# Kernel tuning notes

Measured on AMD Instinct MI355X. Metric: run time of the kernel, lower is better.

## Reference

```python
import jax, jax.numpy as jnp
import numpy as np

B, S, IN_DIM = 8, 4096, 1024
H, D = 16, 64          # num_heads, head_dim (attention_dim = H*D = 1024)
OUT_DIM = 1024
EPS = 1e-6
HI = jax.lax.Precision.HIGHEST


def setup_inputs() -> dict:
    key = jax.random.key(0)
    ks = jax.random.split(key, 9)
    sx = 1.0 / np.sqrt(IN_DIM)
    so = 1.0 / np.sqrt(H * D)
    return {
        "x":  jax.random.normal(ks[0], (B, S, IN_DIM), jnp.float32),
        "wq": jax.random.normal(ks[1], (IN_DIM, H, D), jnp.float32) * sx,
        "bq": jnp.zeros((H, D), jnp.float32),
        "wk": jax.random.normal(ks[2], (IN_DIM, H, D), jnp.float32) * sx,
        "bk": jnp.zeros((H, D), jnp.float32),
        "wv": jax.random.normal(ks[3], (IN_DIM, H, D), jnp.float32) * sx,
        "bv": jnp.zeros((H, D), jnp.float32),
        "wo": jax.random.normal(ks[4], (H, D, OUT_DIM), jnp.float32) * so,
        "bo": jnp.zeros((OUT_DIM,), jnp.float32),
    }


def _feature_map(t):
    return jax.nn.elu(t) + 1.0


def reference(x, wq, bq, wk, bk, wv, bv, wo, bo):
    # QKV projections: [B,S,IN] x [IN,H,D] -> [B,S,H,D]
    q = jnp.einsum('bsi,ihd->bshd', x, wq) + bq
    k = jnp.einsum('bsi,ihd->bshd', x, wk) + bk
    v = jnp.einsum('bsi,ihd->bshd', x, wv) + bv

    Q = _feature_map(q)
    K = _feature_map(k)

    # Faithful to source: KV is an elementwise K*V reduced over seq -> [B,H,D]
    KV = jnp.einsum('bshd,bshd->bhd', K, v, precision=HI)
    Ksum = jnp.sum(K, axis=1)                      # [B,H,D]
    Z = 1.0 / (Q * Ksum[:, None, :, :] + EPS)      # [B,S,H,D]
    attn = Q * KV[:, None, :, :] * Z               # [B,S,H,D]

    # output projection contracts heads and head_dim
    out = jnp.einsum('bshd,hdo->bso', attn, wo) + bo
    return jax.nn.gelu(out)  # flax default gelu is approximate=True
```

## Files before the change

### kernel.cpp

```cpp
#include <hip/hip_runtime.h>


#define SEQ   4096
#define MROWS 32768
#define KDIM  1024
#define HD    1024
#define T32   32

typedef __bf16 bf16x8 __attribute__((ext_vector_type(8)));
typedef float floatx4 __attribute__((ext_vector_type(4)));

__device__ __forceinline__ unsigned short f2bf(float f) {
    unsigned int u = __float_as_uint(f);
    u += 0x7fffu + ((u >> 16) & 1u);
    return (unsigned short)(u >> 16);
}
__device__ __forceinline__ void cvt8(const float* __restrict__ p, unsigned short* d) {
    const float4 a = *(const float4*)p;
    const float4 b = *(const float4*)(p + 4);
    d[0] = f2bf(a.x); d[1] = f2bf(a.y); d[2] = f2bf(a.z); d[3] = f2bf(a.w);
    d[4] = f2bf(b.x); d[5] = f2bf(b.y); d[6] = f2bf(b.z); d[7] = f2bf(b.w);
}

typedef const __attribute__((address_space(1))) unsigned int* gas_t;
typedef __attribute__((address_space(3))) unsigned int* las_t;
__device__ __forceinline__ void async16(const void* g, void* l) {
    __builtin_amdgcn_global_load_lds((gas_t)g, (las_t)l, 16, 0, 0);
}

__global__ __launch_bounds__(256)
void cvt_x(const float* __restrict__ x, unsigned short* __restrict__ xb)
{
    const size_t p = ((size_t)blockIdx.x * 256 + threadIdx.x) * 8;
    union { uint4 u; unsigned short s[8]; } o;
    cvt8(x + p, o.s);
    *(uint4*)(xb + p) = o.u;
}

__global__ __launch_bounds__(256)
void transpose_w(const float* __restrict__ wk, const float* __restrict__ wv,
                 unsigned short* __restrict__ wkT, unsigned short* __restrict__ wvT)
{
    __shared__ alignas(16) unsigned short Ts[64][72];
    const float* W = blockIdx.z ? wv : wk;
    unsigned short* WT = blockIdx.z ? wvT : wkT;
    const int k0 = blockIdx.x * 64, n0 = blockIdx.y * 64;
    const int t = threadIdx.x;
    const int r4 = (t >> 4) * 4, c4 = (t & 15) * 4;
#pragma unroll
    for (int i = 0; i < 4; i++) {
        const float4 f = *(const float4*)(W + (size_t)(k0 + r4 + i) * HD + n0 + c4);
        Ts[c4 + 0][r4 + i] = f2bf(f.x);
        Ts[c4 + 1][r4 + i] = f2bf(f.y);
        Ts[c4 + 2][r4 + i] = f2bf(f.z);
        Ts[c4 + 3][r4 + i] = f2bf(f.w);
    }
    __syncthreads();
    const int rr = t >> 3, cc = (t & 7) * 8;
#pragma unroll
    for (int h = 0; h < 2; h++)
        *(uint4*)(WT + (size_t)(n0 + rr + h * 32) * KDIM + k0 + cc) =
            *(const uint4*)&Ts[rr + h * 32][cc];
}

__global__ __launch_bounds__(512, 1)
void kv_gemm_fast(const unsigned short* __restrict__ xb,
                  const unsigned short* __restrict__ wkT,
                  const unsigned short* __restrict__ wvT,
                  const float* __restrict__ bk, const float* __restrict__ bv,
                  float2* __restrict__ KVZ)
{
    __shared__ alignas(16) unsigned short As[4][256 * 32];
    __shared__ alignas(16) unsigned short Bs[4][256 * 32];

    const int t = threadIdx.x;

    const int id = blockIdx.x;
    const int xcd = id & 7, o = id >> 3;
    const int mtile = xcd * 16 + (o >> 3);
    const int ntile = o & 7;
    const int m0 = mtile * 256;
    const int n0 = ntile * 128;
    const int b  = m0 >> 12;

    const int w = t >> 6, lane = t & 63;
    const int wm = w >> 1, wn = w & 1;
    const int lrow = lane & 15, quad = lane >> 4;

    const int usw = quad ^ ((lrow >> 1) & 3);

    const int srow  = t >> 2;
    const int usrc  = (t & 3) ^ ((t >> 3) & 3);
    const unsigned short* gA0 = xb  + (size_t)(m0 + srow) * KDIM + usrc * 8;
    const unsigned short* gA1 = gA0 + (size_t)128 * KDIM;
    const unsigned short* gBk = wkT + (size_t)(n0 + srow) * KDIM + usrc * 8;
    const unsigned short* gBv = wvT + (size_t)(n0 + srow) * KDIM + usrc * 8;

#define STAGE(c, tk) do {                                                     \
        const int ko_ = (tk) * 32;                                            \
        async16(gA0 + ko_, &As[c][(0 * 512 + t) * 8]);                        \
        async16(gA1 + ko_, &As[c][(1 * 512 + t) * 8]);                        \
        async16(gBk + ko_, &Bs[c][(0 * 512 + t) * 8]);                        \
        async16(gBv + ko_, &Bs[c][(1 * 512 + t) * 8]);                        \
    } while (0)

    STAGE(0, 0);
    STAGE(1, 1);
    STAGE(2, 2);

    floatx4 accK[4][4], accV[4][4];
#pragma unroll
    for (int i = 0; i < 4; i++)
#pragma unroll
        for (int j = 0; j < 4; j++) {
            accK[i][j] = (floatx4){0.f, 0.f, 0.f, 0.f};
            accV[i][j] = (floatx4){0.f, 0.f, 0.f, 0.f};
        }

    asm volatile("s_waitcnt vmcnt(8)" ::: "memory");
    __builtin_amdgcn_s_barrier();

    for (int tk = 0; tk < T32; ++tk) {
        const unsigned short* A = As[tk & 3];
        const unsigned short* B = Bs[tk & 3];

        bf16x8 af[4], bK[4], bV[4];
#pragma unroll
        for (int mi = 0; mi < 4; ++mi)
            af[mi] = *(const bf16x8*)&A[(wm * 64 + mi * 16 + lrow) * 32 + usw * 8];
#pragma unroll
        for (int ni = 0; ni < 4; ++ni) {
            const int br = wn * 64 + ni * 16 + lrow;
            bK[ni] = *(const bf16x8*)&B[ br        * 32 + usw * 8];
            bV[ni] = *(const bf16x8*)&B[(br + 128) * 32 + usw * 8];
        }

        __builtin_amdgcn_s_setprio(1);
#pragma unroll
        for (int mi = 0; mi < 4; ++mi)
#pragma unroll
            for (int ni = 0; ni < 4; ++ni) {
                accK[mi][ni] = __builtin_amdgcn_mfma_f32_16x16x32_bf16(
                    af[mi], bK[ni], accK[mi][ni], 0, 0, 0);
                accV[mi][ni] = __builtin_amdgcn_mfma_f32_16x16x32_bf16(
                    af[mi], bV[ni], accV[mi][ni], 0, 0, 0);
            }
        __builtin_amdgcn_s_setprio(0);

        if (tk + 3 < T32) {
            STAGE((tk + 3) & 3, tk + 3);
            asm volatile("s_waitcnt vmcnt(8)" ::: "memory");
        } else if (tk == T32 - 3) {
            asm volatile("s_waitcnt vmcnt(4)" ::: "memory");
        } else if (tk == T32 - 2) {
            asm volatile("s_waitcnt vmcnt(0)" ::: "memory");
        }
        __builtin_amdgcn_s_barrier();
    }
#undef STAGE

#pragma unroll
    for (int ni = 0; ni < 4; ++ni) {
        const int colw = n0 + wn * 64 + ni * 16 + lrow;
        const float bkf = bk[colw];
        const float bvf = bv[colw];
        float pKV = 0.f, pK = 0.f;
#pragma unroll
        for (int mi = 0; mi < 4; ++mi) {
#pragma unroll
            for (int r = 0; r < 4; ++r) {
                const float kk = accK[mi][ni][r] + bkf;
                const float K  = (kk > 0.f) ? (kk + 1.f) : __expf(kk);
                const float vv = accV[mi][ni][r] + bvf;
                pKV += K * vv;
                pK  += K;
            }
        }
        pKV += __shfl_xor(pKV, 16, 64);
        pKV += __shfl_xor(pKV, 32, 64);
        pK  += __shfl_xor(pK, 16, 64);
        pK  += __shfl_xor(pK, 32, 64);
        if (quad == 0) {
            atomicAdd(&KVZ[b * HD + colw].x, pKV);
            atomicAdd(&KVZ[b * HD + colw].y, pK);
        }
    }
}

__global__ __launch_bounds__(256)
void kv_gemm(const float* __restrict__ x,
             const float* __restrict__ wk, const float* __restrict__ bk,
             const float* __restrict__ wv, const float* __restrict__ bv,
             float2* __restrict__ KVZ)
{
    __shared__ alignas(16) unsigned short As [128][40];
    __shared__ alignas(16) unsigned short BsK[128][40];
    __shared__ alignas(16) unsigned short BsV[128][40];

    const int t = threadIdx.x;
    const int n0 = blockIdx.x * 128;
    const int m0 = blockIdx.y * 128;
    const int b  = m0 >> 12;

    const int wave = t >> 6, lane = t & 63;
    const int wm = wave >> 1, wn = wave & 1;
    const int lrow = lane & 15, quad = lane >> 4;

    floatx4 accK[4][4], accV[4][4];
#pragma unroll
    for (int i = 0; i < 4; i++)
#pragma unroll
        for (int j = 0; j < 4; j++) {
            accK[i][j] = (floatx4){0.f, 0.f, 0.f, 0.f};
            accV[i][j] = (floatx4){0.f, 0.f, 0.f, 0.f};
        }

    const int arow0 = t >> 2, akc = (t & 3) * 8;
    const int bk0 = t >> 4, bnc = (t & 15) * 8;

    for (int k0 = 0; k0 < KDIM; k0 += 32) {
        __syncthreads();
        {
            union { uint4 u; unsigned short s[8]; } ua, ub;
            cvt8(x + (size_t)(m0 + arow0) * KDIM + k0 + akc, ua.s);
            cvt8(x + (size_t)(m0 + arow0 + 64) * KDIM + k0 + akc, ub.s);
            *(uint4*)&As[arow0][akc] = ua.u;
            *(uint4*)&As[arow0 + 64][akc] = ub.u;
        }
        {
            unsigned short k0s[8], k1s[8], v0s[8], v1s[8];
            cvt8(wk + (size_t)(k0 + bk0) * HD + n0 + bnc, k0s);
            cvt8(wk + (size_t)(k0 + bk0 + 16) * HD + n0 + bnc, k1s);
            cvt8(wv + (size_t)(k0 + bk0) * HD + n0 + bnc, v0s);
            cvt8(wv + (size_t)(k0 + bk0 + 16) * HD + n0 + bnc, v1s);
#pragma unroll
            for (int j = 0; j < 8; j++) {
                BsK[bnc + j][bk0]      = k0s[j];
                BsK[bnc + j][bk0 + 16] = k1s[j];
                BsV[bnc + j][bk0]      = v0s[j];
                BsV[bnc + j][bk0 + 16] = v1s[j];
            }
        }
        __syncthreads();

        bf16x8 af[4], bfK[4], bfV[4];
#pragma unroll
        for (int mi = 0; mi < 4; mi++)
            af[mi] = *(const bf16x8*)&As[wm * 64 + mi * 16 + lrow][quad * 8];
#pragma unroll
        for (int ni = 0; ni < 4; ni++) {
            bfK[ni] = *(const bf16x8*)&BsK[wn * 64 + ni * 16 + lrow][quad * 8];
            bfV[ni] = *(const bf16x8*)&BsV[wn * 64 + ni * 16 + lrow][quad * 8];
        }
#pragma unroll
        for (int mi = 0; mi < 4; mi++)
#pragma unroll
            for (int ni = 0; ni < 4; ni++) {
                accK[mi][ni] = __builtin_amdgcn_mfma_f32_16x16x32_bf16(
                    af[mi], bfK[ni], accK[mi][ni], 0, 0, 0);
                accV[mi][ni] = __builtin_amdgcn_mfma_f32_16x16x32_bf16(
                    af[mi], bfV[ni], accV[mi][ni], 0, 0, 0);
            }
    }

#pragma unroll
    for (int ni = 0; ni < 4; ni++) {
        const int colw = n0 + wn * 64 + ni * 16 + lrow;
        const float bkf = bk[colw];
        const float bvf = bv[colw];
        float pKV = 0.f, pK = 0.f;
#pragma unroll
        for (int mi = 0; mi < 4; mi++) {
#pragma unroll
            for (int r = 0; r < 4; r++) {
                const float kk = accK[mi][ni][r] + bkf;
                const float K  = (kk > 0.f) ? (kk + 1.f) : __expf(kk);
                const float vv = accV[mi][ni][r] + bvf;
                pKV += K * vv;
                pK  += K;
            }
        }
        pKV += __shfl_xor(pKV, 16, 64);
        pKV += __shfl_xor(pKV, 32, 64);
        pK  += __shfl_xor(pK, 16, 64);
        pK  += __shfl_xor(pK, 32, 64);
        if (quad == 0) {
            atomicAdd(&KVZ[b * HD + colw].x, pKV);
            atomicAdd(&KVZ[b * HD + colw].y, pK);
        }
    }
}

__global__ __launch_bounds__(256)
void rowgemm_bcast(const float2* __restrict__ KVZ,
                   const float* __restrict__ wo, const float* __restrict__ bo,
                   float* __restrict__ out)
{
    __shared__ float a[1024];
    __shared__ float red[4][64];
    __shared__ float sval[64];
    const int t = threadIdx.x;
    const int b = blockIdx.x;
    const int o0 = blockIdx.y * 64;
    const int s0 = blockIdx.z * 512;

    for (int c = t; c < 1024; c += 256) {
        const float2 z = KVZ[b * HD + c];
        a[c] = z.x / z.y;
    }
    __syncthreads();

    const int cs = t >> 6, oi = t & 63;
    float p = 0.f;
    const int cbeg = cs * 256;
    for (int c = cbeg; c < cbeg + 256; ++c)
        p += a[c] * wo[(size_t)c * HD + o0 + oi];
    red[cs][oi] = p;
    __syncthreads();

    if (t < 64) {
        float v = red[0][t] + red[1][t] + red[2][t] + red[3][t] + bo[o0 + t];
        sval[t] = 0.5f * v *
            (1.f + tanhf(0.7978845608028654f * (v + 0.044715f * v * v * v)));
    }
    __syncthreads();

    const float4 sv4 = *(const float4*)&sval[(t & 15) * 4];
    for (int r = t >> 4; r < 512; r += 16)
        *(float4*)&out[((size_t)(b * SEQ + s0 + r)) * HD + o0 + (t & 15) * 4] = sv4;
}

__global__ __launch_bounds__(256)
void rowgemm(const float2* __restrict__ KVZ,
             const float* __restrict__ wo, const float* __restrict__ bo,
             float* __restrict__ rowf)
{
    __shared__ float a[1024];
    __shared__ float red[4][64];
    const int t = threadIdx.x;
    const int b = blockIdx.x;
    const int o0 = blockIdx.y * 64;

    for (int c = t; c < 1024; c += 256) {
        const float2 z = KVZ[b * HD + c];
        a[c] = z.x / z.y;
    }
    __syncthreads();

    const int cs = t >> 6, oi = t & 63;
    float p = 0.f;
    const int cbeg = cs * 256;
    for (int c = cbeg; c < cbeg + 256; ++c)
        p += a[c] * wo[(size_t)c * HD + o0 + oi];
    red[cs][oi] = p;
    __syncthreads();

    if (t < 64) {
        float v = red[0][t] + red[1][t] + red[2][t] + red[3][t] + bo[o0 + t];
        const float g = 0.5f * v *
            (1.f + tanhf(0.7978845608028654f * (v + 0.044715f * v * v * v)));
        rowf[b * HD + o0 + t] = g;
    }
}

__global__ __launch_bounds__(256)
void broadcast_rows(const float* __restrict__ rowf, float* __restrict__ out)
{
    const size_t idx = (size_t)blockIdx.x * 256 + threadIdx.x;
    const size_t p = idx * 4;
    const int row = (int)(p >> 10);
    const int b = row >> 12;
    const int col = (int)(p & 1023);
    *(float4*)(out + p) = *(const float4*)(rowf + b * HD + col);
}

extern "C" void kernel_launch(void* const* d_in, const int* in_sizes, int n_in,
                              void* d_out, int out_size, void* d_ws, size_t ws_size,
                              hipStream_t stream)
{
    const float* x  = (const float*)d_in[0];
    const float* wk = (const float*)d_in[3];
    const float* bk = (const float*)d_in[4];
    const float* wv = (const float*)d_in[5];
    const float* bv = (const float*)d_in[6];
    const float* wo = (const float*)d_in[7];
    const float* bo = (const float*)d_in[8];
    float* out = (float*)d_out;

    const size_t NEED = (size_t)72 * 1024 * 1024;
    if (ws_size >= NEED) {
        unsigned short* xb  = (unsigned short*)d_ws;
        unsigned short* wkT = (unsigned short*)((char*)d_ws + (67u << 20));
        unsigned short* wvT = (unsigned short*)((char*)d_ws + (69u << 20));
        float2* KVZ = (float2*)((char*)d_ws + (71u << 20));

        hipMemsetAsync(KVZ, 0, 8 * HD * sizeof(float2), stream);
        cvt_x<<<dim3(MROWS * KDIM / 8 / 256), 256, 0, stream>>>(x, xb);
        transpose_w<<<dim3(16, 16, 2), 256, 0, stream>>>(wk, wv, wkT, wvT);
        kv_gemm_fast<<<dim3(1024), 512, 0, stream>>>(xb, wkT, wvT, bk, bv, KVZ);
        rowgemm_bcast<<<dim3(8, 16, 8), 256, 0, stream>>>(KVZ, wo, bo, out);
    } else {
        float2* KVZ = (float2*)d_ws;
        float* rowf = (float*)((char*)d_ws + 65536);
        hipMemsetAsync(KVZ, 0, 8 * HD * sizeof(float2), stream);
        kv_gemm<<<dim3(8, 256), 256, 0, stream>>>(x, wk, bk, wv, bv, KVZ);
        rowgemm<<<dim3(8, 16), 256, 0, stream>>>(KVZ, wo, bo, rowf);
        broadcast_rows<<<dim3((MROWS * HD / 4) / 256), 256, 0, stream>>>(rowf, out);
    }
}
```

Measured before the change: 408.9 us.

## Double-buffer LDS fragment loads in registers and unroll the K-loop by four

Restructures the kv_gemm main loop so that each step's LDS-to-register fragment loads go into a second register set while the MFMAs consume the previous set. This is meant to hide LDS read latency behind matrix-core work. The loop is unrolled four ways with fixed buffer indices and an explicit epilogue. Launch bounds also change to request 2 blocks per CU. That caps registers per thread while the accumulators plus the two fragment sets need many more, so spilling is a risk, and the 128KB of LDS per block probably prevents a second block from being resident anyway.

Result: no change. 405.0 us (-0.9%).

```diff
diff --git a/kernel.cpp b/kernel.cpp
--- a/kernel.cpp
+++ b/kernel.cpp
@@ -63,7 +63,7 @@
             *(const uint4*)&Ts[rr + h * 32][cc];
 }
 
-__global__ __launch_bounds__(512, 1)
+__global__ __launch_bounds__(512, 2)
 void kv_gemm_fast(const unsigned short* __restrict__ xb,
                   const unsigned short* __restrict__ wkT,
                   const unsigned short* __restrict__ wvT,
@@ -104,60 +104,75 @@
         async16(gBv + ko_, &Bs[c][(1 * 512 + t) * 8]);                        \
     } while (0)
 
+    bf16x8 afA[4], bKA[4], bVA[4];
+    bf16x8 afB[4], bKB[4], bVB[4];
+
+#define LOADSET(af_, bK_, bV_, c) do {                                        \
+        _Pragma("unroll")                                                     \
+        for (int mi = 0; mi < 4; ++mi)                                        \
+            af_[mi] = *(const bf16x8*)&As[c][(wm * 64 + mi * 16 + lrow) * 32 + usw * 8]; \
+        _Pragma("unroll")                                                     \
+        for (int ni = 0; ni < 4; ++ni) {                                      \
+            const int br_ = wn * 64 + ni * 16 + lrow;                         \
+            bK_[ni] = *(const bf16x8*)&Bs[c][ br_        * 32 + usw * 8];     \
+            bV_[ni] = *(const bf16x8*)&Bs[c][(br_ + 128) * 32 + usw * 8];     \
+        }                                                                     \
+    } while (0)
+
+#define MFMASET(af_, bK_, bV_) do {                                           \
+        __builtin_amdgcn_s_setprio(1);                                        \
+        _Pragma("unroll")                                                     \
+        for (int mi = 0; mi < 4; ++mi)                                        \
+            _Pragma("unroll")                                                 \
+            for (int ni = 0; ni < 4; ++ni) {                                  \
+                accK[mi][ni] = __builtin_amdgcn_mfma_f32_16x16x32_bf16(       \
+                    af_[mi], bK_[ni], accK[mi][ni], 0, 0, 0);                 \
+                accV[mi][ni] = __builtin_amdgcn_mfma_f32_16x16x32_bf16(       \
+                    af_[mi], bV_[ni], accV[mi][ni], 0, 0, 0);                 \
+            }                                                                 \
+        __builtin_amdgcn_s_setprio(0);                                        \
+    } while (0)
+
+#define WAIT8 asm volatile("s_waitcnt vmcnt(8)" ::: "memory")
+#define BAR   __builtin_amdgcn_s_barrier()
+
+    floatx4 accK[4][4], accV[4][4];
+#pragma unroll
+    for (int i = 0; i < 4; i++)
+#pragma unroll
+        for (int j = 0; j < 4; j++) {
+            accK[i][j] = (floatx4){0.f, 0.f, 0.f, 0.f};
+            accV[i][j] = (floatx4){0.f, 0.f, 0.f, 0.f};
+        }
+
     STAGE(0, 0);
     STAGE(1, 1);
     STAGE(2, 2);
-
-    floatx4 accK[4][4], accV[4][4];
-#pragma unroll
-    for (int i = 0; i < 4; i++)
-#pragma unroll
-        for (int j = 0; j < 4; j++) {
-            accK[i][j] = (floatx4){0.f, 0.f, 0.f, 0.f};
-            accV[i][j] = (floatx4){0.f, 0.f, 0.f, 0.f};
-        }
-
-    asm volatile("s_waitcnt vmcnt(8)" ::: "memory");
-    __builtin_amdgcn_s_barrier();
-
-    for (int tk = 0; tk < T32; ++tk) {
-        const unsigned short* A = As[tk & 3];
-        const unsigned short* B = Bs[tk & 3];
-
-        bf16x8 af[4], bK[4], bV[4];
-#pragma unroll
-        for (int mi = 0; mi < 4; ++mi)
-            af[mi] = *(const bf16x8*)&A[(wm * 64 + mi * 16 + lrow) * 32 + usw * 8];
-#pragma unroll
-        for (int ni = 0; ni < 4; ++ni) {
-            const int br = wn * 64 + ni * 16 + lrow;
-            bK[ni] = *(const bf16x8*)&B[ br        * 32 + usw * 8];
-            bV[ni] = *(const bf16x8*)&B[(br + 128) * 32 + usw * 8];
-        }
-
-        __builtin_amdgcn_s_setprio(1);
-#pragma unroll
-        for (int mi = 0; mi < 4; ++mi)
-#pragma unroll
-            for (int ni = 0; ni < 4; ++ni) {
-                accK[mi][ni] = __builtin_amdgcn_mfma_f32_16x16x32_bf16(
-                    af[mi], bK[ni], accK[mi][ni], 0, 0, 0);
-                accV[mi][ni] = __builtin_amdgcn_mfma_f32_16x16x32_bf16(
-                    af[mi], bV[ni], accV[mi][ni], 0, 0, 0);
-            }
-        __builtin_amdgcn_s_setprio(0);
-
-        if (tk + 3 < T32) {
-            STAGE((tk + 3) & 3, tk + 3);
-            asm volatile("s_waitcnt vmcnt(8)" ::: "memory");
-        } else if (tk == T32 - 3) {
-            asm volatile("s_waitcnt vmcnt(4)" ::: "memory");
-        } else if (tk == T32 - 2) {
-            asm volatile("s_waitcnt vmcnt(0)" ::: "memory");
-        }
-        __builtin_amdgcn_s_barrier();
-    }
+    WAIT8;
+    BAR;
+    LOADSET(afA, bKA, bVA, 0);
+
+    for (int it = 0; it < 7; ++it) {
+        const int tk = it * 4;
+        STAGE(3, tk + 3); WAIT8; BAR; LOADSET(afB, bKB, bVB, 1); MFMASET(afA, bKA, bVA);
+        STAGE(0, tk + 4); WAIT8; BAR; LOADSET(afA, bKA, bVA, 2); MFMASET(afB, bKB, bVB);
+        STAGE(1, tk + 5); WAIT8; BAR; LOADSET(afB, bKB, bVB, 3); MFMASET(afA, bKA, bVA);
+        STAGE(2, tk + 6); WAIT8; BAR; LOADSET(afA, bKA, bVA, 0); MFMASET(afB, bKB, bVB);
+    }
+
+    STAGE(3, 31); WAIT8; BAR;
+    LOADSET(afB, bKB, bVB, 1); MFMASET(afA, bKA, bVA);
+    asm volatile("s_waitcnt vmcnt(4)" ::: "memory"); BAR;
+    LOADSET(afA, bKA, bVA, 2); MFMASET(afB, bKB, bVB);
+    asm volatile("s_waitcnt vmcnt(0)" ::: "memory"); BAR;
+    LOADSET(afB, bKB, bVB, 3); MFMASET(afA, bKA, bVA);
+    MFMASET(afB, bKB, bVB);
+
 #undef STAGE
+#undef LOADSET
+#undef MFMASET
+#undef WAIT8
+#undef BAR
 
 #pragma unroll
     for (int ni = 0; ni < 4; ++ni) {
```

## Split K/V MFMA phases with interleaved staging and merge prep kernels

Applied to the files above, without the earlier changes.

Merges the x conversion and weight transpose kernels into one launch, saving a kernel launch and its tail. Splits each k-step of the KV GEMM main loop into two phases: a K-MFMA phase while the next A tile is staged, and a V-MFMA phase while the next B tile is staged. Barriers and sched_barriers pin the ordering so LDS reads and global loads interleave with the matrix ops, and fewer B fragments are live at once. This adds two extra barriers per iteration and can stall waves if the phases become unbalanced.

After: 401.0 us. No clear change (-1.9%).

```diff
diff --git a/kernel.cpp b/kernel.cpp
--- a/kernel.cpp
+++ b/kernel.cpp
@@ -29,23 +29,23 @@
 }
 
 __global__ __launch_bounds__(256)
-void cvt_x(const float* __restrict__ x, unsigned short* __restrict__ xb)
-{
-    const size_t p = ((size_t)blockIdx.x * 256 + threadIdx.x) * 8;
-    union { uint4 u; unsigned short s[8]; } o;
-    cvt8(x + p, o.s);
-    *(uint4*)(xb + p) = o.u;
-}
-
-__global__ __launch_bounds__(256)
-void transpose_w(const float* __restrict__ wk, const float* __restrict__ wv,
-                 unsigned short* __restrict__ wkT, unsigned short* __restrict__ wvT)
+void prep(const float* __restrict__ x, unsigned short* __restrict__ xb,
+          const float* __restrict__ wk, const float* __restrict__ wv,
+          unsigned short* __restrict__ wkT, unsigned short* __restrict__ wvT)
 {
     __shared__ alignas(16) unsigned short Ts[64][72];
-    const float* W = blockIdx.z ? wv : wk;
-    unsigned short* WT = blockIdx.z ? wvT : wkT;
-    const int k0 = blockIdx.x * 64, n0 = blockIdx.y * 64;
     const int t = threadIdx.x;
+    if (blockIdx.x < 16384) {
+        const size_t p = ((size_t)blockIdx.x * 256 + t) * 8;
+        union { uint4 u; unsigned short s[8]; } o;
+        cvt8(x + p, o.s);
+        *(uint4*)(xb + p) = o.u;
+        return;
+    }
+    const int bid = blockIdx.x - 16384;
+    const float* W = (bid >> 8) ? wv : wk;
+    unsigned short* WT = (bid >> 8) ? wvT : wkT;
+    const int k0 = (bid & 15) * 64, n0 = ((bid >> 4) & 15) * 64;
     const int r4 = (t >> 4) * 4, c4 = (t & 15) * 4;
 #pragma unroll
     for (int i = 0; i < 4; i++) {
@@ -96,17 +96,22 @@
     const unsigned short* gBk = wkT + (size_t)(n0 + srow) * KDIM + usrc * 8;
     const unsigned short* gBv = wvT + (size_t)(n0 + srow) * KDIM + usrc * 8;
 
-#define STAGE(c, tk) do {                                                     \
+#define STAGE_A(c, tk) do {                                                   \
         const int ko_ = (tk) * 32;                                            \
         async16(gA0 + ko_, &As[c][(0 * 512 + t) * 8]);                        \
         async16(gA1 + ko_, &As[c][(1 * 512 + t) * 8]);                        \
+    } while (0)
+#define STAGE_B(c, tk) do {                                                   \
+        const int ko_ = (tk) * 32;                                            \
         async16(gBk + ko_, &Bs[c][(0 * 512 + t) * 8]);                        \
         async16(gBv + ko_, &Bs[c][(1 * 512 + t) * 8]);                        \
     } while (0)
-
-    STAGE(0, 0);
-    STAGE(1, 1);
-    STAGE(2, 2);
+#define BAR   __builtin_amdgcn_s_barrier()
+#define SCHED __builtin_amdgcn_sched_barrier(0)
+
+    STAGE_A(0, 0); STAGE_B(0, 0);
+    STAGE_A(1, 1); STAGE_B(1, 1);
+    STAGE_A(2, 2); STAGE_B(2, 2);
 
     floatx4 accK[4][4], accV[4][4];
 #pragma unroll
@@ -118,46 +123,60 @@
         }
 
     asm volatile("s_waitcnt vmcnt(8)" ::: "memory");
-    __builtin_amdgcn_s_barrier();
+    BAR;
 
     for (int tk = 0; tk < T32; ++tk) {
-        const unsigned short* A = As[tk & 3];
-        const unsigned short* B = Bs[tk & 3];
-
-        bf16x8 af[4], bK[4], bV[4];
+        const int c = tk & 3;
+        const unsigned short* A = As[c];
+        const unsigned short* B = Bs[c];
+        const int nx = (tk + 3) & 3;
+
+        bf16x8 af[4], bK[4];
 #pragma unroll
         for (int mi = 0; mi < 4; ++mi)
             af[mi] = *(const bf16x8*)&A[(wm * 64 + mi * 16 + lrow) * 32 + usw * 8];
 #pragma unroll
-        for (int ni = 0; ni < 4; ++ni) {
-            const int br = wn * 64 + ni * 16 + lrow;
-            bK[ni] = *(const bf16x8*)&B[ br        * 32 + usw * 8];
-            bV[ni] = *(const bf16x8*)&B[(br + 128) * 32 + usw * 8];
-        }
-
+        for (int ni = 0; ni < 4; ++ni)
+            bK[ni] = *(const bf16x8*)&B[(wn * 64 + ni * 16 + lrow) * 32 + usw * 8];
+        if (tk + 3 < T32) STAGE_A(nx, tk + 3);
+        BAR; SCHED;
         __builtin_amdgcn_s_setprio(1);
 #pragma unroll
         for (int mi = 0; mi < 4; ++mi)
 #pragma unroll
-            for (int ni = 0; ni < 4; ++ni) {
+            for (int ni = 0; ni < 4; ++ni)
                 accK[mi][ni] = __builtin_amdgcn_mfma_f32_16x16x32_bf16(
                     af[mi], bK[ni], accK[mi][ni], 0, 0, 0);
-                accV[mi][ni] = __builtin_amdgcn_mfma_f32_16x16x32_bf16(
-                    af[mi], bV[ni], accV[mi][ni], 0, 0, 0);
-            }
         __builtin_amdgcn_s_setprio(0);
-
+        SCHED; BAR;
+
+        bf16x8 bV[4];
+#pragma unroll
+        for (int ni = 0; ni < 4; ++ni)
+            bV[ni] = *(const bf16x8*)&B[(128 + wn * 64 + ni * 16 + lrow) * 32 + usw * 8];
         if (tk + 3 < T32) {
-            STAGE((tk + 3) & 3, tk + 3);
+            STAGE_B(nx, tk + 3);
             asm volatile("s_waitcnt vmcnt(8)" ::: "memory");
         } else if (tk == T32 - 3) {
             asm volatile("s_waitcnt vmcnt(4)" ::: "memory");
         } else if (tk == T32 - 2) {
             asm volatile("s_waitcnt vmcnt(0)" ::: "memory");
         }
-        __builtin_amdgcn_s_barrier();
-    }
-#undef STAGE
+        BAR; SCHED;
+        __builtin_amdgcn_s_setprio(1);
+#pragma unroll
+        for (int mi = 0; mi < 4; ++mi)
+#pragma unroll
+            for (int ni = 0; ni < 4; ++ni)
+                accV[mi][ni] = __builtin_amdgcn_mfma_f32_16x16x32_bf16(
+                    af[mi], bV[ni], accV[mi][ni], 0, 0, 0);
+        __builtin_amdgcn_s_setprio(0);
+        SCHED; BAR;
+    }
+#undef STAGE_A
+#undef STAGE_B
+#undef BAR
+#undef SCHED
 
 #pragma unroll
     for (int ni = 0; ni < 4; ++ni) {
@@ -395,8 +414,7 @@
         float2* KVZ = (float2*)((char*)d_ws + (71u << 20));
 
         hipMemsetAsync(KVZ, 0, 8 * HD * sizeof(float2), stream);
-        cvt_x<<<dim3(MROWS * KDIM / 8 / 256), 256, 0, stream>>>(x, xb);
-        transpose_w<<<dim3(16, 16, 2), 256, 0, stream>>>(wk, wv, wkT, wvT);
+        prep<<<dim3(16384 + 512), 256, 0, stream>>>(x, xb, wk, wv, wkT, wvT);
         kv_gemm_fast<<<dim3(1024), 512, 0, stream>>>(xb, wkT, wvT, bk, bv, KVZ);
         rowgemm_bcast<<<dim3(8, 16, 8), 256, 0, stream>>>(KVZ, wo, bo, out);
     } else {
```
